# Performance work log

Hardware: AMD Instinct MI355X
Metric: run time of the kernel (lower is better)

Reference implementation:

```python
import jax, jax.numpy as jnp
import numpy as np

K = 16  # max sampled neighbors per node (from __init__)
INVALID = -1.0  # sentinel below any uniform noise value in [0, 1)


def setup_inputs() -> dict:
    key = jax.random.key(0)
    k1, k2, k3, k4, k5 = jax.random.split(key, 5)
    B, N, D = 8, 2048, 128
    s = jax.random.normal(k1, (B, N, D), dtype=jnp.float32)
    noise = jax.random.uniform(k2, (B, N, N), dtype=jnp.float32)
    adj_allowed = jax.random.randint(k3, (B, N, N), 0, 2, dtype=jnp.int32)
    active_mask = jax.random.randint(k4, (B, N), 0, 2, dtype=jnp.int32)
    act_mask = jax.random.randint(k5, (B, N), 0, 2, dtype=jnp.int32)
    return {"s": s, "noise": noise, "adj_allowed": adj_allowed,
            "active_mask": active_mask, "act_mask": act_mask}


def reference(s, noise, adj_allowed, active_mask, act_mask):
    # s: [B,N,D]; noise: [B,N,N] uniform keys; masks int32.
    B, N, D = s.shape
    # candidate j for node (b,i): active_mask[b,j] > 0 AND adj_allowed[b,i,j] > 0
    valid = (active_mask[:, None, :] > 0) & (adj_allowed > 0)          # [B,N,N]
    scores = jnp.where(valid, noise, INVALID)                           # [B,N,N]
    # Gumbel/top-k of uniform keys == uniform random subset of size K (randperm[:K])
    top_vals, top_idx = jax.lax.top_k(scores, K)                        # [B,N,K]
    sel_valid = (top_vals >= 0.0) & (act_mask[:, :, None] > 0)          # drop padding / inactive rows
    b_idx = jnp.arange(B)[:, None, None]
    i_idx = jnp.arange(N)[None, :, None]
    gate = jnp.zeros((B, N, N), dtype=jnp.float32)
    gate = gate.at[b_idx, i_idx, top_idx].set(sel_valid.astype(jnp.float32))
    # normalized weights, clamped denominator as in torch.clamp(min=1.0)
    w = gate / jnp.maximum(gate.sum(axis=-1, keepdims=True), 1.0)       # [B,N,N]
    ctx = jnp.einsum('bij,bjd->bid', w, s)                              # [B,N,D]
    return ctx, gate, w
```

## Files before the change

kernel.cpp:

```cpp
#include <hip/hip_runtime.h>

#define NN 2048
#define DD 128
#define KK 16
#define DIRTY 0xFFFFFFFFFFFFFFFFull

typedef float f4 __attribute__((ext_vector_type(4)));

__device__ __forceinline__ unsigned long long packkey(float v, int j) {
    unsigned long long k = ((unsigned long long)(__float_as_uint(v) + 1u) << 11)
                         | (unsigned int)(2047 - j);
    return (v >= 0.0f) ? k : 0ull;
}

__global__ __launch_bounds__(64) void rc_topk_kernel(
    const float* __restrict__ s,
    const float* __restrict__ noise,
    const int*   __restrict__ adj,
    const int*   __restrict__ active,
    const int*   __restrict__ act,
    float* __restrict__ ctx,
    float* __restrict__ gate,
    float* __restrict__ w)
{
    __shared__ float sc[NN];

    const int lane = threadIdx.x;
    const int row  = blockIdx.x;
    const int b    = row >> 11;
    const long long rowoff = (long long)row * NN;

    if (act[row] == 0) {
        const f4 z4 = (f4)0.0f;
        #pragma unroll
        for (int t = 0; t < 8; ++t) {
            const int j = t * 256 + lane * 4;
            __builtin_nontemporal_store(z4, (f4*)&gate[rowoff + j]);
            __builtin_nontemporal_store(z4, (f4*)&w[rowoff + j]);
        }
        *(float2*)&ctx[(long long)row * DD + lane * 2] = make_float2(0.f, 0.f);
        return;
    }

    float b1v = -4.0f, b2v = -4.0f; int b1j = 0, b2j = 0;
    #pragma unroll
    for (int t = 0; t < 8; ++t) {
        const int j = t * 256 + lane * 4;
        const float4 nz = *(const float4*)&noise[rowoff + j];
        const int4   ad = *(const int4*)&adj[rowoff + j];
        const int4   am = *(const int4*)&active[b * NN + j];
        const float v0 = (ad.x > 0 && am.x > 0) ? nz.x : -1.0f;
        const float v1 = (ad.y > 0 && am.y > 0) ? nz.y : -1.0f;
        const float v2 = (ad.z > 0 && am.z > 0) ? nz.z : -1.0f;
        const float v3 = (ad.w > 0 && am.w > 0) ? nz.w : -1.0f;
        *(float4*)&sc[j] = make_float4(v0, v1, v2, v3);
        if (v0 > b1v) { b2v = b1v; b2j = b1j; b1v = v0; b1j = j;     }
        else if (v0 > b2v) { b2v = v0; b2j = j;     }
        if (v1 > b1v) { b2v = b1v; b2j = b1j; b1v = v1; b1j = j + 1; }
        else if (v1 > b2v) { b2v = v1; b2j = j + 1; }
        if (v2 > b1v) { b2v = b1v; b2j = b1j; b1v = v2; b1j = j + 2; }
        else if (v2 > b2v) { b2v = v2; b2j = j + 2; }
        if (v3 > b1v) { b2v = b1v; b2j = b1j; b1v = v3; b1j = j + 3; }
        else if (v3 > b2v) { b2v = v3; b2j = j + 3; }
    }
    unsigned long long k1 = packkey(b1v, b1j);
    unsigned long long k2 = packkey(b2v, b2j);

    int cnt = 0, myj = -1;
    float2 acc  = make_float2(0.f, 0.f);
    float2 pend = make_float2(0.f, 0.f);
    for (int k = 0; k < KK; ++k) {
        unsigned long long rk = k1;
        #pragma unroll
        for (int off = 32; off > 0; off >>= 1) {
            const unsigned long long o = __shfl_xor(rk, off, 64);
            if (o > rk) rk = o;
        }
        if (rk == 0ull) break;
        acc.x += pend.x; acc.y += pend.y;
        const int rj = 2047 - (int)((unsigned int)rk & 0x7FFu);
        pend = *(const float2*)&s[((long long)(b * NN + rj)) * DD + lane * 2];
        if (lane == k) myj = rj;
        ++cnt;
        if (k1 == rk) {
            sc[rj] = -2.0f;
            if (k2 != DIRTY) { k1 = k2; k2 = DIRTY; }
            else {
                float c1v = -4.0f, c2v = -4.0f; int c1j = 0, c2j = 0;
                #pragma unroll
                for (int t = 0; t < 8; ++t) {
                    const int j = t * 256 + lane * 4;
                    const float4 q = *(const float4*)&sc[j];
                    if (q.x > c1v) { c2v = c1v; c2j = c1j; c1v = q.x; c1j = j;     }
                    else if (q.x > c2v) { c2v = q.x; c2j = j;     }
                    if (q.y > c1v) { c2v = c1v; c2j = c1j; c1v = q.y; c1j = j + 1; }
                    else if (q.y > c2v) { c2v = q.y; c2j = j + 1; }
                    if (q.z > c1v) { c2v = c1v; c2j = c1j; c1v = q.z; c1j = j + 2; }
                    else if (q.z > c2v) { c2v = q.z; c2j = j + 2; }
                    if (q.w > c1v) { c2v = c1v; c2j = c1j; c1v = q.w; c1j = j + 3; }
                    else if (q.w > c2v) { c2v = q.w; c2j = j + 3; }
                }
                k1 = packkey(c1v, c1j);
                k2 = packkey(c2v, c2j);
            }
        }
    }
    acc.x += pend.x; acc.y += pend.y;

    __syncthreads();
    const float inv = 1.0f / (float)(cnt > 1 ? cnt : 1);

    const float4 z4h = make_float4(0.f, 0.f, 0.f, 0.f);
    #pragma unroll
    for (int t = 0; t < 8; ++t) *(float4*)&sc[t * 256 + lane * 4] = z4h;
    __syncthreads();
    if (lane < cnt) sc[myj] = 1.0f;
    __syncthreads();

    #pragma unroll
    for (int t = 0; t < 8; ++t) {
        const int j = t * 256 + lane * 4;
        const f4 g = *(const f4*)&sc[j];
        __builtin_nontemporal_store(g, (f4*)&gate[rowoff + j]);
        const f4 wv = g * inv;
        __builtin_nontemporal_store(wv, (f4*)&w[rowoff + j]);
    }

    *(float2*)&ctx[(long long)row * DD + lane * 2] = make_float2(acc.x * inv, acc.y * inv);
}

extern "C" void kernel_launch(void* const* d_in, const int* in_sizes, int n_in,
                              void* d_out, int out_size, void* d_ws, size_t ws_size,
                              hipStream_t stream) {
    const float* s      = (const float*)d_in[0];
    const float* noise  = (const float*)d_in[1];
    const int*   adj    = (const int*)d_in[2];
    const int*   active = (const int*)d_in[3];
    const int*   act    = (const int*)d_in[4];

    const int B = in_sizes[3] / NN;
    const long long ctxN  = (long long)B * NN * DD;
    const long long gateN = (long long)B * NN * NN;

    float* ctxp = (float*)d_out;
    float* gatep = ctxp + ctxN;
    float* wp = gatep + gateN;

    rc_topk_kernel<<<B * NN, 64, 0, stream>>>(s, noise, adj, active, act, ctxp, gatep, wp);
}
```

Baseline: 74.88 us.

## Replace LDS score buffer with per-lane selection bitmask and float argmax

Removes the 8KB shared-memory score array. Selected positions are now tracked in a 32-bit per-lane bitmask, and candidate values are recomputed from global noise/adj/active when a lane needs a rescan. The wave reduction becomes a float max plus a ballot-based tie-break instead of a 64-bit packed-key shuffle, and the LDS zero/scatter and barriers before the gate store are gone. Occupancy is raised via launch_bounds(64,8). The cost is re-reading global memory (likely L2/L1 hits) on each rescan.

```diff
diff --git a/kernel.cpp b/kernel.cpp
--- a/kernel.cpp
+++ b/kernel.cpp
@@ -3,17 +3,10 @@
 #define NN 2048
 #define DD 128
 #define KK 16
-#define DIRTY 0xFFFFFFFFFFFFFFFFull
 
 typedef float f4 __attribute__((ext_vector_type(4)));
 
-__device__ __forceinline__ unsigned long long packkey(float v, int j) {
-    unsigned long long k = ((unsigned long long)(__float_as_uint(v) + 1u) << 11)
-                         | (unsigned int)(2047 - j);
-    return (v >= 0.0f) ? k : 0ull;
-}
-
-__global__ __launch_bounds__(64) void rc_topk_kernel(
+__global__ __launch_bounds__(64, 8) void rc_topk_kernel(
     const float* __restrict__ s,
     const float* __restrict__ noise,
     const int*   __restrict__ adj,
@@ -23,8 +16,6 @@
     float* __restrict__ gate,
     float* __restrict__ w)
 {
-    __shared__ float sc[NN];
-
     const int lane = threadIdx.x;
     const int row  = blockIdx.x;
     const int b    = row >> 11;
@@ -42,7 +33,7 @@
         return;
     }
 
-    float b1v = -4.0f, b2v = -4.0f; int b1j = 0, b2j = 0;
+    float k1v = -4.0f, k2v = -4.0f; int k1j = 0, k2j = 0;
     #pragma unroll
     for (int t = 0; t < 8; ++t) {
         const int j = t * 256 + lane * 4;
@@ -53,74 +44,84 @@
         const float v1 = (ad.y > 0 && am.y > 0) ? nz.y : -1.0f;
         const float v2 = (ad.z > 0 && am.z > 0) ? nz.z : -1.0f;
         const float v3 = (ad.w > 0 && am.w > 0) ? nz.w : -1.0f;
-        *(float4*)&sc[j] = make_float4(v0, v1, v2, v3);
-        if (v0 > b1v) { b2v = b1v; b2j = b1j; b1v = v0; b1j = j;     }
-        else if (v0 > b2v) { b2v = v0; b2j = j;     }
-        if (v1 > b1v) { b2v = b1v; b2j = b1j; b1v = v1; b1j = j + 1; }
-        else if (v1 > b2v) { b2v = v1; b2j = j + 1; }
-        if (v2 > b1v) { b2v = b1v; b2j = b1j; b1v = v2; b1j = j + 2; }
-        else if (v2 > b2v) { b2v = v2; b2j = j + 2; }
-        if (v3 > b1v) { b2v = b1v; b2j = b1j; b1v = v3; b1j = j + 3; }
-        else if (v3 > b2v) { b2v = v3; b2j = j + 3; }
+        if (v0 > k1v) { k2v = k1v; k2j = k1j; k1v = v0; k1j = j;     }
+        else if (v0 > k2v) { k2v = v0; k2j = j;     }
+        if (v1 > k1v) { k2v = k1v; k2j = k1j; k1v = v1; k1j = j + 1; }
+        else if (v1 > k2v) { k2v = v1; k2j = j + 1; }
+        if (v2 > k1v) { k2v = k1v; k2j = k1j; k1v = v2; k1j = j + 2; }
+        else if (v2 > k2v) { k2v = v2; k2j = j + 2; }
+        if (v3 > k1v) { k2v = k1v; k2j = k1j; k1v = v3; k1j = j + 3; }
+        else if (v3 > k2v) { k2v = v3; k2j = j + 3; }
     }
-    unsigned long long k1 = packkey(b1v, b1j);
-    unsigned long long k2 = packkey(b2v, b2j);
+    bool k2dirty = false;
+    unsigned int selmask = 0;
 
-    int cnt = 0, myj = -1;
+    int cnt = 0;
     float2 acc  = make_float2(0.f, 0.f);
     float2 pend = make_float2(0.f, 0.f);
     for (int k = 0; k < KK; ++k) {
-        unsigned long long rk = k1;
+        float mv = k1v;
         #pragma unroll
-        for (int off = 32; off > 0; off >>= 1) {
-            const unsigned long long o = __shfl_xor(rk, off, 64);
-            if (o > rk) rk = o;
+        for (int off = 32; off; off >>= 1) mv = fmaxf(mv, __shfl_xor(mv, off, 64));
+        if (mv < 0.0f) break;
+        const unsigned long long tied = __ballot(k1v == mv);
+        int rj;
+        if (__popcll(tied) == 1) {
+            rj = __shfl(k1j, (int)__builtin_ctzll(tied), 64);
+        } else {
+            int pj = (k1v == mv) ? k1j : 0x7FFFFFFF;
+            #pragma unroll
+            for (int off = 32; off; off >>= 1) {
+                const int o = __shfl_xor(pj, off, 64);
+                pj = o < pj ? o : pj;
+            }
+            rj = pj;
         }
-        if (rk == 0ull) break;
         acc.x += pend.x; acc.y += pend.y;
-        const int rj = 2047 - (int)((unsigned int)rk & 0x7FFu);
         pend = *(const float2*)&s[((long long)(b * NN + rj)) * DD + lane * 2];
-        if (lane == k) myj = rj;
         ++cnt;
-        if (k1 == rk) {
-            sc[rj] = -2.0f;
-            if (k2 != DIRTY) { k1 = k2; k2 = DIRTY; }
+        if (k1v == mv && k1j == rj) {
+            selmask |= 1u << (((rj >> 8) << 2) | (rj & 3));
+            if (!k2dirty) { k1v = k2v; k1j = k2j; k2dirty = true; }
             else {
                 float c1v = -4.0f, c2v = -4.0f; int c1j = 0, c2j = 0;
                 #pragma unroll
                 for (int t = 0; t < 8; ++t) {
                     const int j = t * 256 + lane * 4;
-                    const float4 q = *(const float4*)&sc[j];
-                    if (q.x > c1v) { c2v = c1v; c2j = c1j; c1v = q.x; c1j = j;     }
-                    else if (q.x > c2v) { c2v = q.x; c2j = j;     }
-                    if (q.y > c1v) { c2v = c1v; c2j = c1j; c1v = q.y; c1j = j + 1; }
-                    else if (q.y > c2v) { c2v = q.y; c2j = j + 1; }
-                    if (q.z > c1v) { c2v = c1v; c2j = c1j; c1v = q.z; c1j = j + 2; }
-                    else if (q.z > c2v) { c2v = q.z; c2j = j + 2; }
-                    if (q.w > c1v) { c2v = c1v; c2j = c1j; c1v = q.w; c1j = j + 3; }
-                    else if (q.w > c2v) { c2v = q.w; c2j = j + 3; }
+                    const float4 nz = *(const float4*)&noise[rowoff + j];
+                    const int4   ad = *(const int4*)&adj[rowoff + j];
+                    const int4   am = *(const int4*)&active[b * NN + j];
+                    const unsigned mb = selmask >> (t * 4);
+                    const float v0 = (ad.x > 0 && am.x > 0 && !(mb & 1u)) ? nz.x : -1.0f;
+                    const float v1 = (ad.y > 0 && am.y > 0 && !(mb & 2u)) ? nz.y : -1.0f;
+                    const float v2 = (ad.z > 0 && am.z > 0 && !(mb & 4u)) ? nz.z : -1.0f;
+                    const float v3 = (ad.w > 0 && am.w > 0 && !(mb & 8u)) ? nz.w : -1.0f;
+                    if (v0 > c1v) { c2v = c1v; c2j = c1j; c1v = v0; c1j = j;     }
+                    else if (v0 > c2v) { c2v = v0; c2j = j;     }
+                    if (v1 > c1v) { c2v = c1v; c2j = c1j; c1v = v1; c1j = j + 1; }
+                    else if (v1 > c2v) { c2v = v1; c2j = j + 1; }
+                    if (v2 > c1v) { c2v = c1v; c2j = c1j; c1v = v2; c1j = j + 2; }
+                    else if (v2 > c2v) { c2v = v2; c2j = j + 2; }
+                    if (v3 > c1v) { c2v = c1v; c2j = c1j; c1v = v3; c1j = j + 3; }
+                    else if (v3 > c2v) { c2v = v3; c2j = j + 3; }
                 }
-                k1 = packkey(c1v, c1j);
-                k2 = packkey(c2v, c2j);
+                k1v = c1v; k1j = c1j; k2v = c2v; k2j = c2j; k2dirty = false;
             }
         }
     }
     acc.x += pend.x; acc.y += pend.y;
 
-    __syncthreads();
     const float inv = 1.0f / (float)(cnt > 1 ? cnt : 1);
-
-    const float4 z4h = make_float4(0.f, 0.f, 0.f, 0.f);
-    #pragma unroll
-    for (int t = 0; t < 8; ++t) *(float4*)&sc[t * 256 + lane * 4] = z4h;
-    __syncthreads();
-    if (lane < cnt) sc[myj] = 1.0f;
-    __syncthreads();
 
     #pragma unroll
     for (int t = 0; t < 8; ++t) {
         const int j = t * 256 + lane * 4;
-        const f4 g = *(const f4*)&sc[j];
+        const unsigned mb = selmask >> (t * 4);
+        f4 g;
+        g.x = (mb & 1u) ? 1.0f : 0.0f;
+        g.y = (mb & 2u) ? 1.0f : 0.0f;
+        g.z = (mb & 4u) ? 1.0f : 0.0f;
+        g.w = (mb & 8u) ? 1.0f : 0.0f;
         __builtin_nontemporal_store(g, (f4*)&gate[rowoff + j]);
         const f4 wv = g * inv;
         __builtin_nontemporal_store(wv, (f4*)&w[rowoff + j]);
```

Result: slower. 117.1 us (+56.4%).
